# Kernel optimization log

Hardware: AMD Instinct MI355X
Metric: run time of the kernel (lower is better)

The kernel has to match this reference:

```python
import jax, jax.numpy as jnp
import numpy as np

COUNTS = [1536, 8192, 16384, 24576, 12288, 1024, 512, 512, 256, 128, 128]
OFFS = np.concatenate([[0], np.cumsum(COUNTS)]).astype(int).tolist()
N = OFFS[-1]          # 65536 atoms total, sorted by degree
MAX_DEG = 10
BATCH = 2048          # fixed GraphGather batch size
F_IN = 75
GC = 256
DENSE = 512
N_TASKS = 12
N_CLASSES = 2
BN_EPS = 1e-3         # keras BatchNormalization default epsilon


def _graph_conv(x, deg_adjs, w0, wself, wneigh, b):
    # deepchem GraphConv: per-degree (self @ Wself + sum_neighbors @ Wneigh + b), relu
    outs = [x[OFFS[0]:OFFS[1]] @ w0 + b[0]]  # degree-0 atoms: self transform only
    for d in range(1, MAX_DEG + 1):
        self_atoms = x[OFFS[d]:OFFS[d + 1]]            # [n_d, F]
        neigh = x[deg_adjs[d - 1]].sum(axis=1)         # gather [n_d, d, F] -> sum -> [n_d, F]
        outs.append(self_atoms @ wself[d - 1] + neigh @ wneigh[d - 1] + b[d])
    return jax.nn.relu(jnp.concatenate(outs, axis=0))


def _graph_pool(x, deg_adjs):
    # deepchem GraphPool: elementwise max over {self} U neighbors, per degree
    outs = [x[OFFS[0]:OFFS[1]]]  # degree-0 atoms pass through
    for d in range(1, MAX_DEG + 1):
        self_atoms = x[OFFS[d]:OFFS[d + 1]]
        outs.append(jnp.maximum(self_atoms, x[deg_adjs[d - 1]].max(axis=1)))
    return jnp.concatenate(outs, axis=0)


def _bn(x, g, bta, m, v):
    # inference-mode BatchNormalization (training=False -> moving stats)
    return g * (x - m) * jax.lax.rsqrt(v + BN_EPS) + bta


def setup_inputs():
    key = jax.random.key(0)
    ks = iter(jax.random.split(key, 64))
    inp = {}
    inp["atom_features"] = jax.random.normal(next(ks), (N, F_IN), jnp.float32)
    inp["degree_slice"] = jnp.asarray(
        np.stack([np.array(OFFS[:-1]), np.array(COUNTS)], axis=1), jnp.int32)
    # each molecule gets exactly N/BATCH atoms so no GraphGather segment is empty
    inp["membership"] = jax.random.permutation(
        next(ks), jnp.arange(N, dtype=jnp.int32) % BATCH)
    inp["n_samples"] = BATCH
    for d in range(1, MAX_DEG + 1):
        inp["deg_adj_%d" % d] = jax.random.randint(
            next(ks), (COUNTS[d], d), 0, N, jnp.int32)

    def lin(k, fi, fo):
        return jax.random.normal(k, (fi, fo), jnp.float32) * np.float32(1.0 / np.sqrt(fi))

    for li, fi in [(1, F_IN), (2, GC)]:
        inp["gc%d_w0" % li] = lin(next(ks), fi, GC)
        inp["gc%d_wself" % li] = jnp.stack([lin(next(ks), fi, GC) for _ in range(MAX_DEG)])
        inp["gc%d_wneigh" % li] = jnp.stack([lin(next(ks), fi, GC) for _ in range(MAX_DEG)])
        inp["gc%d_b" % li] = jnp.zeros((MAX_DEG + 1, GC), jnp.float32)
    for bi, dim in [(1, GC), (2, GC), (3, DENSE)]:
        inp["bn%d_gamma" % bi] = jnp.ones((dim,), jnp.float32)
        inp["bn%d_beta" % bi] = jnp.zeros((dim,), jnp.float32)
        inp["bn%d_mean" % bi] = jnp.zeros((dim,), jnp.float32)
        inp["bn%d_var" % bi] = jnp.ones((dim,), jnp.float32)
    inp["dense_w"] = lin(next(ks), GC, DENSE)
    inp["dense_b"] = jnp.zeros((DENSE,), jnp.float32)
    inp["out_w"] = lin(next(ks), 2 * DENSE, N_TASKS * N_CLASSES)
    inp["out_b"] = jnp.zeros((N_TASKS * N_CLASSES,), jnp.float32)
    return inp


def reference(atom_features, degree_slice, membership, n_samples,
              deg_adj_1, deg_adj_2, deg_adj_3, deg_adj_4, deg_adj_5,
              deg_adj_6, deg_adj_7, deg_adj_8, deg_adj_9, deg_adj_10,
              gc1_w0, gc1_wself, gc1_wneigh, gc1_b,
              gc2_w0, gc2_wself, gc2_wneigh, gc2_b,
              bn1_gamma, bn1_beta, bn1_mean, bn1_var,
              bn2_gamma, bn2_beta, bn2_mean, bn2_var,
              bn3_gamma, bn3_beta, bn3_mean, bn3_var,
              dense_w, dense_b, out_w, out_b):
    deg_adjs = [deg_adj_1, deg_adj_2, deg_adj_3, deg_adj_4, deg_adj_5,
                deg_adj_6, deg_adj_7, deg_adj_8, deg_adj_9, deg_adj_10]
    h = _graph_conv(atom_features, deg_adjs, gc1_w0, gc1_wself, gc1_wneigh, gc1_b)
    h = _bn(h, bn1_gamma, bn1_beta, bn1_mean, bn1_var)
    h = _graph_pool(h, deg_adjs)
    h = _graph_conv(h, deg_adjs, gc2_w0, gc2_wself, gc2_wneigh, gc2_b)
    h = _bn(h, bn2_gamma, bn2_beta, bn2_mean, bn2_var)
    h = _graph_pool(h, deg_adjs)
    h = jax.nn.relu(h @ dense_w + dense_b)
    h = _bn(h, bn3_gamma, bn3_beta, bn3_mean, bn3_var)
    # GraphGather: tanh(concat(segment_sum, segment_max))
    ssum = jax.ops.segment_sum(h, membership, num_segments=BATCH)
    smax = jax.ops.segment_max(h, membership, num_segments=BATCH)
    fp = jnp.tanh(jnp.concatenate([ssum, smax], axis=1))   # [BATCH, 2*DENSE]
    logits = (fp @ out_w + out_b).reshape(BATCH, N_TASKS, N_CLASSES)[:n_samples]
    probs = jax.nn.softmax(logits, axis=-1)
    return probs, logits, fp
```

## Files before the change

kernel.cpp:

```cpp
#include <hip/hip_runtime.h>
#include <hip/hip_fp16.h>
#include <math.h>

#define NATOMS 65536

typedef _Float16 f16_t;
typedef __attribute__((ext_vector_type(8))) _Float16 half8;
typedef __attribute__((ext_vector_type(4))) float f32x4;

__constant__ int c_offs[12] = {0,1536,9728,26112,50688,62976,64000,64512,65024,65280,65408,65536};

struct Adj { const int* p[10]; };

__device__ __forceinline__ int seg_of(int row) {
    int s = 0;
#pragma unroll
    for (int i = 1; i <= 10; ++i) s += (row >= c_offs[i]) ? 1 : 0;
    return s;
}

__device__ __forceinline__ void glds16(const f16_t* g, f16_t* l) {
    __builtin_amdgcn_global_load_lds(
        (const __attribute__((address_space(1))) unsigned int*)g,
        (__attribute__((address_space(3))) unsigned int*)l,
        16, 0, 0);
}

__device__ __forceinline__ half8 max8(half8 a, half8 b) {
    half8 r;
#pragma unroll
    for (int e = 0; e < 8; ++e) r[e] = (a[e] >= b[e]) ? a[e] : b[e];
    return r;
}


__global__ void pack_cvt(const float* __restrict__ g1w0, const float* __restrict__ g1ws,
                         const float* __restrict__ g1wn,
                         const float* __restrict__ g2w0, const float* __restrict__ g2ws,
                         const float* __restrict__ g2wn,
                         const float* __restrict__ dw, const float* __restrict__ ow,
                         f16_t* __restrict__ W1p, f16_t* __restrict__ W2p,
                         f16_t* __restrict__ Wdp, f16_t* __restrict__ Wop,
                         int* __restrict__ counts,
                         const float* __restrict__ xf, f16_t* __restrict__ xq) {
    if (blockIdx.x >= 8384) {
        int idx = (blockIdx.x - 8384) * 256 + threadIdx.x;
        int r = idx / 12;
        int cc = idx - r * 12;
        int c = cc << 3;
        f16_t o[8];
#pragma unroll
        for (int e = 0; e < 8; ++e)
            o[e] = (c + e < 75) ? (f16_t)xf[(size_t)r*75 + c + e] : (f16_t)0.f;
        *(uint4*)(xq + (size_t)r*96 + c) = *(uint4*)o;
        return;
    }
    int idx = blockIdx.x * 256 + threadIdx.x;
    if (idx < 2048) counts[idx] = 0;
    if (idx < 540672) {
        int j = idx & 7, lane = (idx >> 3) & 63;
        int kb = (idx >> 9) % 6;
        int rest = idx / (512 * 6);
        int ni = rest & 15, s = rest >> 4;
        int k = kb * 32 + (lane >> 4) * 8 + j;
        int n = ni * 16 + (lane & 15);
        float v = 0.f;
        if (k < 75) v = (s == 0) ? g1w0[k*256 + n] : g1ws[((s-1)*75 + k)*256 + n];
        else if (k >= 96 && k < 171 && s > 0) v = g1wn[((s-1)*75 + (k-96))*256 + n];
        W1p[idx] = (f16_t)v;
    } else if (idx < 1982464) {
        int i2 = idx - 540672;
        int j = i2 & 7, lane = (i2 >> 3) & 63;
        int kb = (i2 >> 9) & 15;
        int rest = i2 >> 13;
        int ni = rest & 15, s = rest >> 4;
        int k = kb * 32 + (lane >> 4) * 8 + j;
        int n = ni * 16 + (lane & 15);
        float v = 0.f;
        if (k < 256) v = (s == 0) ? g2w0[k*256 + n] : g2ws[((s-1)*256 + k)*256 + n];
        else if (s > 0) v = g2wn[((s-1)*256 + (k-256))*256 + n];
        W2p[i2] = (f16_t)v;
    } else if (idx < 2113536) {
        int i2 = idx - 1982464;
        int j = i2 & 7, lane = (i2 >> 3) & 63;
        int kb = (i2 >> 9) & 7;
        int ni = (i2 >> 12) & 31;
        int k = kb * 32 + (lane >> 4) * 8 + j;
        int n = ni * 16 + (lane & 15);
        Wdp[i2] = (f16_t)dw[(size_t)k*512 + n];
    } else {
        int i2 = idx - 2113536;
        int j = i2 & 7, lane = (i2 >> 3) & 63;
        int kb = (i2 >> 9) & 31;
        int ni = i2 >> 14;
        int k = kb * 32 + (lane >> 4) * 8 + j;
        int n = ni * 16 + (lane & 15);
        Wop[i2] = (n < 24) ? (f16_t)ow[k*24 + n] : (f16_t)0.f;
    }
}

template<int D, int LD>
__device__ __forceinline__ void gathD(float* v, const f16_t* __restrict__ src,
                                      const int* __restrict__ ap, int c) {
    int rows[D];
#pragma unroll
    for (int j = 0; j < D; ++j) rows[j] = ap[j];
    uint4 raw[D];
#pragma unroll
    for (int j = 0; j < D; ++j) raw[j] = *(const uint4*)(src + (size_t)rows[j]*LD + c);
#pragma unroll
    for (int j = 0; j < D; ++j) {
        const f16_t* u = (const f16_t*)&raw[j];
#pragma unroll
        for (int e = 0; e < 8; ++e) v[e] += (float)u[e];
    }
}

template<int LD>
__device__ __forceinline__ void gath_sum(float* v, const f16_t* __restrict__ src,
                                         const int* __restrict__ ap, int s, int c) {
    switch (s) {
        case 1:  gathD<1,LD>(v,src,ap,c);  break;
        case 2:  gathD<2,LD>(v,src,ap,c);  break;
        case 3:  gathD<3,LD>(v,src,ap,c);  break;
        case 4:  gathD<4,LD>(v,src,ap,c);  break;
        case 5:  gathD<5,LD>(v,src,ap,c);  break;
        case 6:  gathD<6,LD>(v,src,ap,c);  break;
        case 7:  gathD<7,LD>(v,src,ap,c);  break;
        case 8:  gathD<8,LD>(v,src,ap,c);  break;
        case 9:  gathD<9,LD>(v,src,ap,c);  break;
        case 10: gathD<10,LD>(v,src,ap,c); break;
        default: break;
    }
}

template<int D, int LD>
__device__ __forceinline__ void gathD_pk(half8& v, const f16_t* __restrict__ src,
                                         const int* __restrict__ ap, int c) {
    int rows[D];
#pragma unroll
    for (int j = 0; j < D; ++j) rows[j] = ap[j];
    half8 raw[D];
#pragma unroll
    for (int j = 0; j < D; ++j) raw[j] = *(const half8*)(src + (size_t)rows[j]*LD + c);
#pragma unroll
    for (int j = 0; j < D; ++j) v = max8(v, raw[j]);
}

template<int LD>
__device__ __forceinline__ void gath_max(half8& v, const f16_t* __restrict__ src,
                                         const int* __restrict__ ap, int s, int c) {
    switch (s) {
        case 1:  gathD_pk<1,LD>(v,src,ap,c);  break;
        case 2:  gathD_pk<2,LD>(v,src,ap,c);  break;
        case 3:  gathD_pk<3,LD>(v,src,ap,c);  break;
        case 4:  gathD_pk<4,LD>(v,src,ap,c);  break;
        case 5:  gathD_pk<5,LD>(v,src,ap,c);  break;
        case 6:  gathD_pk<6,LD>(v,src,ap,c);  break;
        case 7:  gathD_pk<7,LD>(v,src,ap,c);  break;
        case 8:  gathD_pk<8,LD>(v,src,ap,c);  break;
        case 9:  gathD_pk<9,LD>(v,src,ap,c);  break;
        case 10: gathD_pk<10,LD>(v,src,ap,c); break;
        default: break;
    }
}

__global__ __launch_bounds__(256) void nbsum_sc(const f16_t* __restrict__ xq,
                                                f16_t* __restrict__ NBX, Adj adj,
                                                const int* __restrict__ mem,
                                                int* __restrict__ counts,
                                                int* __restrict__ slots) {
    if (blockIdx.x >= 3072) {
        int i = (blockIdx.x - 3072) * 256 + threadIdx.x;
        int s = mem[i];
        int p = atomicAdd(&counts[s], 1);
        if (p < 32) slots[s*32 + p] = i;
        return;
    }
    int idx = blockIdx.x * 256 + threadIdx.x;
    int r = (int)((unsigned)idx / 12u);
    int cc = idx - r * 12;
    int c = cc << 3;
    int s = seg_of(r);
    float v[8];
#pragma unroll
    for (int e = 0; e < 8; ++e) v[e] = 0.f;
    if (s > 0)
        gath_sum<96>(v, xq, adj.p[s-1] + (size_t)(r - c_offs[s]) * s, s, c);
    f16_t o[8];
#pragma unroll
    for (int e = 0; e < 8; ++e) o[e] = (f16_t)v[e];
    *(uint4*)(NBX + (size_t)(r>>4)*1536 + (c>>5)*512 + ((c>>3)&3)*128 + (r&15)*8) = *(uint4*)o;
}

template<bool BLOB>
__global__ __launch_bounds__(256) void pool_k(const f16_t* __restrict__ H,
                                              f16_t* __restrict__ P, Adj adj) {
    int idx = blockIdx.x * 256 + threadIdx.x;
    int r = idx >> 5;
    int c = (idx & 31) << 3;
    int s = seg_of(r);
    half8 v = *(const half8*)(H + (size_t)r*256 + c);
    if (s > 0)
        gath_max<256>(v, H, adj.p[s-1] + (size_t)(r - c_offs[s]) * s, s, c);
    if (BLOB)
        *(half8*)(P + (size_t)(r>>4)*4096 + (c>>5)*512 + ((c>>3)&3)*128 + (r&15)*8) = v;
    else
        *(half8*)(P + (size_t)r*256 + c) = v;
}

__global__ __launch_bounds__(256) void nbsum_k(const f16_t* __restrict__ P,
                                               f16_t* __restrict__ NB, Adj adj) {
    int idx = blockIdx.x * 256 + threadIdx.x;
    int r = idx >> 5;
    int c = (idx & 31) << 3;
    int s = seg_of(r);
    float v[8];
#pragma unroll
    for (int e = 0; e < 8; ++e) v[e] = 0.f;
    if (s > 0)
        gath_sum<256>(v, P, adj.p[s-1] + (size_t)(r - c_offs[s]) * s, s, c);
    f16_t o[8];
#pragma unroll
    for (int e = 0; e < 8; ++e) o[e] = (f16_t)v[e];
    *(uint4*)(NB + (size_t)(r>>4)*4096 + (c>>5)*512 + ((c>>3)&3)*128 + (r&15)*8) = *(uint4*)o;
}

template<int NKB, int KSPB, int LDA, int NKBA1, int NY, int N, bool SEG>
__global__ __launch_bounds__(512, 2)
void gemm256(const f16_t* __restrict__ A0, const f16_t* __restrict__ A1,
             const f16_t* __restrict__ Wp,
             const float* __restrict__ bias,
             const float* __restrict__ bng, const float* __restrict__ bnb,
             const float* __restrict__ bnm, const float* __restrict__ bnv,
             f16_t* __restrict__ C)
{
    constexpr int NT  = NKB;
    constexpr int NNT = N / 16;
    __shared__ f16_t sm[32768];

    const int t = threadIdx.x;
    const int lane = t & 63, w = t >> 6;
    const int wm = w >> 2, wn = w & 3;
    const int quad = lane >> 4, l16 = lane & 15;
    const int id = blockIdx.x;
    const int xi = id / NY, y = id - xi * NY;
    const int r0 = xi * 256;
    const int n0 = y * 256;
    const int rtg = r0 >> 4;
    const int nbase = n0 >> 4;
    const int segB = SEG ? seg_of(r0) : 0;
    const bool strad = SEG && (seg_of(r0 + 255) != segB);
    const int segw = SEG ? seg_of(r0 + wm*128) : 0;

    f32x4 acc[8][4];
#pragma unroll
    for (int mi = 0; mi < 8; ++mi)
#pragma unroll
        for (int ni = 0; ni < 4; ++ni) acc[mi][ni] = (f32x4){0.f,0.f,0.f,0.f};

    size_t aoff[2];
#pragma unroll
    for (int i = 0; i < 2; ++i)
        aoff[i] = (size_t)(r0 + (w*2 + i)*16 + l16) * LDA + quad*8;

    auto stage = [&](int kb, int buf) {
        f16_t* bb = sm + buf*16384;
#pragma unroll
        for (int i = 0; i < 2; ++i) {
            const int rt = w*2 + i;
            if constexpr (KSPB > 0) {
                if (kb < KSPB)
                    glds16(A0 + (size_t)kb*32 + aoff[i], bb + rt*512);
                else
                    glds16(A1 + ((size_t)(rtg + rt)*NKBA1 + (kb - KSPB))*512 + lane*8,
                           bb + rt*512);
            } else {
                glds16(A1 + ((size_t)(rtg + rt)*NKBA1 + kb)*512 + lane*8,
                       bb + rt*512);
            }
            glds16(Wp + ((size_t)(segB*NNT + nbase + rt)*NKB + kb)*512 + lane*8,
                   bb + 8192 + rt*512);
        }
    };

    stage(0, 0);
    __syncthreads();

    for (int kt = 0; kt < NT; ++kt) {
        const int buf = kt & 1;
        if (kt + 1 < NT) stage(kt + 1, buf ^ 1);
        const f16_t* bb = sm + buf*16384;

        half8 bfr[4];
        if (strad) {
#pragma unroll
            for (int ni = 0; ni < 4; ++ni)
                bfr[ni] = *(const half8*)(Wp +
                    ((size_t)(segw*NNT + nbase + wn*4 + ni)*NKB + kt)*512 + lane*8);
        } else {
#pragma unroll
            for (int ni = 0; ni < 4; ++ni)
                bfr[ni] = *(const half8*)(bb + 8192 + (wn*4 + ni)*512 + lane*8);
        }

#pragma unroll
        for (int ph = 0; ph < 4; ++ph) {
            half8 a[2];
#pragma unroll
            for (int m2 = 0; m2 < 2; ++m2)
                a[m2] = *(const half8*)(bb + (wm*8 + ph*2 + m2)*512 + lane*8);
#pragma unroll
            for (int m2 = 0; m2 < 2; ++m2)
#pragma unroll
                for (int ni = 0; ni < 4; ++ni)
                    acc[ph*2 + m2][ni] = __builtin_amdgcn_mfma_f32_16x16x32_f16(
                        a[m2], bfr[ni], acc[ph*2 + m2][ni], 0, 0, 0);
        }
        __syncthreads();
    }

    f16_t* eps = sm;
#pragma unroll
    for (int s = 0; s < 4; ++s) {
        if (wm == (s >> 1)) {
#pragma unroll
            for (int ni = 0; ni < 4; ++ni) {
                const int lcol = wn*64 + ni*16 + l16;
                const int col = n0 + lcol;
                const float scale = bng[col] * rsqrtf(bnv[col] + 1e-3f);
                const float shift = bnb[col] - bnm[col] * scale;
                const float bv = bias[(SEG ? segw*N : 0) + col];
#pragma unroll
                for (int m2 = 0; m2 < 4; ++m2) {
                    const int mi = (s & 1)*4 + m2;
                    const int rowb = m2*16 + quad*4;
#pragma unroll
                    for (int rr = 0; rr < 4; ++rr) {
                        float v = acc[mi][ni][rr] + bv;
                        v = fmaxf(v, 0.f);
                        v = fmaf(v, scale, shift);
                        eps[(rowb + rr)*264 + lcol] = (f16_t)v;
                    }
                }
            }
        }
        __syncthreads();
#pragma unroll
        for (int k = 0; k < 4; ++k) {
            int idx = k*512 + t;
            int row = idx >> 5, ch = idx & 31;
            *(uint4*)(C + (size_t)(r0 + s*64 + row)*N + n0 + ch*8) =
                *(const uint4*)&eps[row*264 + ch*8];
        }
        __syncthreads();
    }
}

__global__ __launch_bounds__(256, 2)
void gemm_dir(const f16_t* __restrict__ A, const f16_t* __restrict__ Wp,
              const float* __restrict__ bias,
              const float* __restrict__ bng, const float* __restrict__ bnb,
              const float* __restrict__ bnm, const float* __restrict__ bnv,
              f16_t* __restrict__ C)
{
    constexpr int NKB = 8, N = 512;
    __shared__ f16_t eps[128*136];
    const int t = threadIdx.x, lane = t & 63, w = t >> 6;
    const int wm = w >> 1, wn = w & 1;
    const int quad = lane >> 4, l16 = lane & 15;
    const int id = blockIdx.x;
    const int xcd = id & 7;
    const int j = id >> 3;
    const int xi = xcd * 64 + (j >> 2);
    const int y = j & 3;
    const int r0 = xi * 128, n0 = y * 128;
    const int rt0 = (r0 >> 4) + wm*4;
    const int nt0 = (n0 >> 4) + wn*4;

    f32x4 acc[4][4];
#pragma unroll
    for (int mi = 0; mi < 4; ++mi)
#pragma unroll
        for (int ni = 0; ni < 4; ++ni) acc[mi][ni] = (f32x4){0.f,0.f,0.f,0.f};

    const f16_t* ap = A  + (size_t)rt0 * NKB * 512 + lane*8;
    const f16_t* bp = Wp + (size_t)nt0 * NKB * 512 + lane*8;

    half8 aA[4], bA[4], aB[4], bB[4];
#pragma unroll
    for (int i = 0; i < 4; ++i) {
        aA[i] = *(const half8*)(ap + ((size_t)i*NKB + 0)*512);
        bA[i] = *(const half8*)(bp + ((size_t)i*NKB + 0)*512);
    }
#pragma unroll
    for (int kb = 0; kb < NKB; kb += 2) {
        if (kb + 1 < NKB) {
#pragma unroll
            for (int i = 0; i < 4; ++i) {
                aB[i] = *(const half8*)(ap + ((size_t)i*NKB + kb + 1)*512);
                bB[i] = *(const half8*)(bp + ((size_t)i*NKB + kb + 1)*512);
            }
        }
#pragma unroll
        for (int mi = 0; mi < 4; ++mi)
#pragma unroll
            for (int ni = 0; ni < 4; ++ni)
                acc[mi][ni] = __builtin_amdgcn_mfma_f32_16x16x32_f16(
                    aA[mi], bA[ni], acc[mi][ni], 0, 0, 0);
        if (kb + 2 < NKB) {
#pragma unroll
            for (int i = 0; i < 4; ++i) {
                aA[i] = *(const half8*)(ap + ((size_t)i*NKB + kb + 2)*512);
                bA[i] = *(const half8*)(bp + ((size_t)i*NKB + kb + 2)*512);
            }
        }
        if (kb + 1 < NKB) {
#pragma unroll
            for (int mi = 0; mi < 4; ++mi)
#pragma unroll
                for (int ni = 0; ni < 4; ++ni)
                    acc[mi][ni] = __builtin_amdgcn_mfma_f32_16x16x32_f16(
                        aB[mi], bB[ni], acc[mi][ni], 0, 0, 0);
        }
    }

#pragma unroll
    for (int ni = 0; ni < 4; ++ni) {
        const int lcol = wn*64 + ni*16 + l16;
        const int col = n0 + lcol;
        const float scale = bng[col] * rsqrtf(bnv[col] + 1e-3f);
        const float shift = bnb[col] - bnm[col] * scale;
        const float bv = bias[col];
#pragma unroll
        for (int mi = 0; mi < 4; ++mi) {
            const int rowb = wm*64 + mi*16 + quad*4;
#pragma unroll
            for (int rr = 0; rr < 4; ++rr) {
                float v = acc[mi][ni][rr] + bv;
                v = fmaxf(v, 0.f);
                v = fmaf(v, scale, shift);
                eps[(rowb + rr)*136 + lcol] = (f16_t)v;
            }
        }
    }
    __syncthreads();
#pragma unroll
    for (int k2 = 0; k2 < 8; ++k2) {
        int idx = k2*256 + t;
        int row = idx >> 4, ch = idx & 15;
        *(uint4*)(C + (size_t)(r0 + row)*N + n0 + ch*8) =
            *(const uint4*)&eps[row*136 + ch*8];
    }
}

__global__ __launch_bounds__(256)
void reduce_k(const f16_t* __restrict__ H3, const int* __restrict__ slots,
              float* __restrict__ fp) {
    __shared__ float shs[3][512];
    __shared__ float shm[3][512];
    int s = blockIdx.x;
    int t = threadIdx.x;
    int w = t >> 6, l = t & 63;
    int c = l * 8;
    const int* sl = slots + s*32 + w*8;
    float sm[8], mx[8];
#pragma unroll
    for (int e = 0; e < 8; ++e) { sm[e] = 0.f; mx[e] = -INFINITY; }
#pragma unroll
    for (int i = 0; i < 8; ++i) {
        int a = sl[i];
        uint4 raw = *(const uint4*)(H3 + (size_t)a*512 + c);
        const f16_t* u = (const f16_t*)&raw;
#pragma unroll
        for (int e = 0; e < 8; ++e) {
            float f = (float)u[e];
            sm[e] += f;
            mx[e] = fmaxf(mx[e], f);
        }
    }
    if (w) {
        *(float4*)&shs[w-1][c]   = *(float4*)&sm[0];
        *(float4*)&shs[w-1][c+4] = *(float4*)&sm[4];
        *(float4*)&shm[w-1][c]   = *(float4*)&mx[0];
        *(float4*)&shm[w-1][c+4] = *(float4*)&mx[4];
    }
    __syncthreads();
    if (w == 0) {
#pragma unroll
        for (int j = 0; j < 3; ++j)
#pragma unroll
            for (int e = 0; e < 8; ++e) {
                sm[e] += shs[j][c+e];
                mx[e] = fmaxf(mx[e], shm[j][c+e]);
            }
        float o1[8], o2[8];
#pragma unroll
        for (int e = 0; e < 8; ++e) {
            o1[e] = tanhf(sm[e]); o2[e] = tanhf(mx[e]);
        }
        float* fr = fp + (size_t)s*1024;
        *(float4*)(fr + c)       = *(float4*)&o1[0];
        *(float4*)(fr + c + 4)   = *(float4*)&o1[4];
        *(float4*)(fr + 512 + c)     = *(float4*)&o2[0];
        *(float4*)(fr + 512 + c + 4) = *(float4*)&o2[4];
    }
}

__global__ __launch_bounds__(64)
void final_mfma(const float* __restrict__ fp, const f16_t* __restrict__ Wop,
                const float* __restrict__ out_b,
                float* __restrict__ probs, float* __restrict__ logits) {
    const int t = threadIdx.x;
    const int lane = t & 63;
    const int quad = lane >> 4, l16 = lane & 15;
    const int r0 = blockIdx.x * 16;

    f32x4 acc[2];
#pragma unroll
    for (int ni = 0; ni < 2; ++ni) acc[ni] = (f32x4){0.f,0.f,0.f,0.f};

    const size_t rowoff = (size_t)(r0 + l16) * 1024 + quad*8;
    size_t boff[2];
#pragma unroll
    for (int ni = 0; ni < 2; ++ni)
        boff[ni] = (size_t)ni * 32 * 512 + lane*8;

    auto loadA = [&](half8& a, int kb) {
        const float* src = fp + rowoff + kb*32;
        float4 u0 = *(const float4*)(src);
        float4 u1 = *(const float4*)(src + 4);
        half8 h;
        h[0] = (f16_t)u0.x; h[1] = (f16_t)u0.y; h[2] = (f16_t)u0.z; h[3] = (f16_t)u0.w;
        h[4] = (f16_t)u1.x; h[5] = (f16_t)u1.y; h[6] = (f16_t)u1.z; h[7] = (f16_t)u1.w;
        a = h;
    };
    auto loadB = [&](half8* b, int kb) {
#pragma unroll
        for (int ni = 0; ni < 2; ++ni) b[ni] = *(const half8*)(Wop + boff[ni] + (size_t)kb*512);
    };
    auto domfma = [&](half8& a, half8* b) {
#pragma unroll
        for (int ni = 0; ni < 2; ++ni)
            acc[ni] = __builtin_amdgcn_mfma_f32_16x16x32_f16(a, b[ni], acc[ni], 0, 0, 0);
    };

    half8 a0, b0[2], a1, b1[2];
    loadA(a0, 0); loadB(b0, 0);
#pragma unroll
    for (int kb = 0; kb < 32; kb += 2) {
        loadA(a1, kb + 1); loadB(b1, kb + 1);
        domfma(a0, b0);
        if (kb + 2 < 32) { loadA(a0, kb + 2); loadB(b0, kb + 2); }
        domfma(a1, b1);
    }

#pragma unroll
    for (int ni = 0; ni < 2; ++ni) {
        const int c = ni*16 + l16;
        const bool ok = (c < 24);
        const float bv = ok ? out_b[c] : 0.f;
#pragma unroll
        for (int r = 0; r < 4; ++r) {
            float lg = acc[ni][r] + bv;
            float lp = __shfl_xor(lg, 1);
            float m = fmaxf(lg, lp);
            float e  = expf(lg - m);
            float ep = expf(lp - m);
            float pr = e / (e + ep);
            if (ok) {
                int row = r0 + quad*4 + r;
                logits[(size_t)row*24 + c] = lg;
                probs[(size_t)row*24 + c]  = pr;
            }
        }
    }
}

extern "C" void kernel_launch(void* const* d_in, const int* in_sizes, int n_in,
                              void* d_out, int out_size, void* d_ws, size_t ws_size,
                              hipStream_t stream) {
    const float* atom       = (const float*)d_in[0];
    const int*   membership = (const int*)  d_in[2];
    Adj adj;
    for (int d = 0; d < 10; ++d) adj.p[d] = (const int*)d_in[4+d];
    const float* gc1_w0     = (const float*)d_in[14];
    const float* gc1_wself  = (const float*)d_in[15];
    const float* gc1_wneigh = (const float*)d_in[16];
    const float* gc1_b      = (const float*)d_in[17];
    const float* gc2_w0     = (const float*)d_in[18];
    const float* gc2_wself  = (const float*)d_in[19];
    const float* gc2_wneigh = (const float*)d_in[20];
    const float* gc2_b      = (const float*)d_in[21];
    const float* bn1g = (const float*)d_in[22]; const float* bn1b = (const float*)d_in[23];
    const float* bn1m = (const float*)d_in[24]; const float* bn1v = (const float*)d_in[25];
    const float* bn2g = (const float*)d_in[26]; const float* bn2b = (const float*)d_in[27];
    const float* bn2m = (const float*)d_in[28]; const float* bn2v = (const float*)d_in[29];
    const float* bn3g = (const float*)d_in[30]; const float* bn3b = (const float*)d_in[31];
    const float* bn3m = (const float*)d_in[32]; const float* bn3v = (const float*)d_in[33];
    const float* dense_w = (const float*)d_in[34];
    const float* dense_b = (const float*)d_in[35];
    const float* out_w   = (const float*)d_in[36];
    const float* out_b   = (const float*)d_in[37];

    f16_t* wsb = (f16_t*)d_ws;
    f16_t* xq    = wsb;
    f16_t* NBX   = wsb + 6291456;
    f16_t* H1b   = wsb + 12582912;
    f16_t* P1rm  = wsb + 29360128;
    f16_t* NB2b  = wsb + 46137344;
    f16_t* H2b   = H1b;
    f16_t* P2bl  = NB2b;
    f16_t* H3b   = H1b;
    f16_t* W1p   = wsb + 62914560;
    f16_t* W2p   = wsb + 63455232;
    f16_t* Wdp   = wsb + 64897024;
    f16_t* Wop   = wsb + 65028096;
    int*  counts = (int*)(wsb + 65060864);
    int*  slots  = counts + 2048;

    float* outp   = (float*)d_out;
    float* probs  = outp;
    float* logits = outp + 49152;
    float* fp     = outp + 98304;

    pack_cvt<<<11456, 256, 0, stream>>>(gc1_w0, gc1_wself, gc1_wneigh,
                                        gc2_w0, gc2_wself, gc2_wneigh,
                                        dense_w, out_w,
                                        W1p, W2p, Wdp, Wop, counts,
                                        atom, xq);

    nbsum_sc<<<3328, 256, 0, stream>>>(xq, NBX, adj, membership, counts, slots);
    gemm256<6,3,96,3,1,256,true><<<256, 512, 0, stream>>>(
        xq, NBX, W1p, gc1_b, bn1g, bn1b, bn1m, bn1v, H1b);
    pool_k<false><<<(NATOMS*32)/256, 256, 0, stream>>>(H1b, P1rm, adj);

    nbsum_k<<<(NATOMS*32)/256, 256, 0, stream>>>(P1rm, NB2b, adj);
    gemm256<16,8,256,8,1,256,true><<<256, 512, 0, stream>>>(
        P1rm, NB2b, W2p, gc2_b, bn2g, bn2b, bn2m, bn2v, H2b);
    pool_k<true><<<(NATOMS*32)/256, 256, 0, stream>>>(H2b, P2bl, adj);

    gemm_dir<<<2048, 256, 0, stream>>>(
        P2bl, Wdp, dense_b, bn3g, bn3b, bn3m, bn3v, H3b);

    reduce_k<<<2048, 256, 0, stream>>>(H3b, slots, fp);

    final_mfma<<<128, 64, 0, stream>>>(fp, Wop, out_b, probs, logits);
}
```

Before: 338.5 us.

## Replace LDS-staged 256x256 graph-conv GEMM with direct-register 128x128 tiles

Both graph-conv GEMMs switch from a 512-thread kernel with 256x256 tiles, double-buffered through LDS via global_load_lds, to a 256-thread kernel with 128x128 tiles. Each wave now loads its A and B fragments straight from global memory into registers, double-buffered in registers. Blocks are mapped by XCD so neighbouring row tiles share an L2. Because every degree-segment boundary is a multiple of 128, a tile never spans two segments, so the per-wave weight reload path for straddling tiles goes away. The cost is more global and L2 traffic, since operands are no longer shared through LDS across waves.

```diff
diff --git a/kernel.cpp b/kernel.cpp
--- a/kernel.cpp
+++ b/kernel.cpp
@@ -17,13 +17,6 @@
 #pragma unroll
     for (int i = 1; i <= 10; ++i) s += (row >= c_offs[i]) ? 1 : 0;
     return s;
-}
-
-__device__ __forceinline__ void glds16(const f16_t* g, f16_t* l) {
-    __builtin_amdgcn_global_load_lds(
-        (const __attribute__((address_space(1))) unsigned int*)g,
-        (__attribute__((address_space(3))) unsigned int*)l,
-        16, 0, 0);
 }
 
 __device__ __forceinline__ half8 max8(half8 a, half8 b) {
@@ -226,134 +219,106 @@
     *(uint4*)(NB + (size_t)(r>>4)*4096 + (c>>5)*512 + ((c>>3)&3)*128 + (r&15)*8) = *(uint4*)o;
 }
 
-template<int NKB, int KSPB, int LDA, int NKBA1, int NY, int N, bool SEG>
-__global__ __launch_bounds__(512, 2)
-void gemm256(const f16_t* __restrict__ A0, const f16_t* __restrict__ A1,
+template<int NKB, int KSPB, int LDA, int NKBA1, int N, bool SEG>
+__global__ __launch_bounds__(256, 2)
+void gemm_gc(const f16_t* __restrict__ A0, const f16_t* __restrict__ A1,
              const f16_t* __restrict__ Wp,
              const float* __restrict__ bias,
              const float* __restrict__ bng, const float* __restrict__ bnb,
              const float* __restrict__ bnm, const float* __restrict__ bnv,
              f16_t* __restrict__ C)
 {
-    constexpr int NT  = NKB;
     constexpr int NNT = N / 16;
-    __shared__ f16_t sm[32768];
-
-    const int t = threadIdx.x;
-    const int lane = t & 63, w = t >> 6;
-    const int wm = w >> 2, wn = w & 3;
+    constexpr int NYL = N / 128;
+    __shared__ f16_t eps[128*136];
+    const int t = threadIdx.x, lane = t & 63, w = t >> 6;
+    const int wm = w >> 1, wn = w & 1;
     const int quad = lane >> 4, l16 = lane & 15;
     const int id = blockIdx.x;
-    const int xi = id / NY, y = id - xi * NY;
-    const int r0 = xi * 256;
-    const int n0 = y * 256;
-    const int rtg = r0 >> 4;
-    const int nbase = n0 >> 4;
-    const int segB = SEG ? seg_of(r0) : 0;
-    const bool strad = SEG && (seg_of(r0 + 255) != segB);
-    const int segw = SEG ? seg_of(r0 + wm*128) : 0;
-
-    f32x4 acc[8][4];
-#pragma unroll
-    for (int mi = 0; mi < 8; ++mi)
+    const int xcd = id & 7;
+    const int j = id >> 3;
+    const int xi = xcd * 64 + j / NYL;
+    const int y = j % NYL;
+    const int r0 = xi * 128, n0 = y * 128;
+    const int rt0 = (r0 >> 4) + wm*4;
+    const int nt0 = (n0 >> 4) + wn*4;
+    const int seg = SEG ? seg_of(r0) : 0;
+
+    f32x4 acc[4][4];
+#pragma unroll
+    for (int mi = 0; mi < 4; ++mi)
 #pragma unroll
         for (int ni = 0; ni < 4; ++ni) acc[mi][ni] = (f32x4){0.f,0.f,0.f,0.f};
 
-    size_t aoff[2];
-#pragma unroll
-    for (int i = 0; i < 2; ++i)
-        aoff[i] = (size_t)(r0 + (w*2 + i)*16 + l16) * LDA + quad*8;
-
-    auto stage = [&](int kb, int buf) {
-        f16_t* bb = sm + buf*16384;
-#pragma unroll
-        for (int i = 0; i < 2; ++i) {
-            const int rt = w*2 + i;
-            if constexpr (KSPB > 0) {
-                if (kb < KSPB)
-                    glds16(A0 + (size_t)kb*32 + aoff[i], bb + rt*512);
-                else
-                    glds16(A1 + ((size_t)(rtg + rt)*NKBA1 + (kb - KSPB))*512 + lane*8,
-                           bb + rt*512);
-            } else {
-                glds16(A1 + ((size_t)(rtg + rt)*NKBA1 + kb)*512 + lane*8,
-                       bb + rt*512);
+    const f16_t* bpW = Wp + ((size_t)(seg*NNT + nt0) * NKB) * 512 + lane*8;
+    const f16_t* apB = A1 + (size_t)rt0 * NKBA1 * 512 + lane*8;
+    const f16_t* apR = A0 + (size_t)(r0 + wm*64 + l16) * LDA + quad*8;
+
+    auto loadA = [&](half8& dst, int mi, int kb) {
+        if (kb < KSPB)
+            dst = *(const half8*)(apR + (size_t)(mi*16) * LDA + kb*32);
+        else
+            dst = *(const half8*)(apB + ((size_t)mi*NKBA1 + (kb - KSPB))*512);
+    };
+    auto loadB = [&](half8& dst, int ni, int kb) {
+        dst = *(const half8*)(bpW + ((size_t)ni*NKB + kb)*512);
+    };
+
+    half8 aA[4], bA[4], aB[4], bB[4];
+#pragma unroll
+    for (int i = 0; i < 4; ++i) { loadA(aA[i], i, 0); loadB(bA[i], i, 0); }
+#pragma unroll
+    for (int kb = 0; kb < NKB; kb += 2) {
+        if (kb + 1 < NKB) {
+#pragma unroll
+            for (int i = 0; i < 4; ++i) { loadA(aB[i], i, kb + 1); loadB(bB[i], i, kb + 1); }
+        }
+#pragma unroll
+        for (int mi = 0; mi < 4; ++mi)
+#pragma unroll
+            for (int ni = 0; ni < 4; ++ni)
+                acc[mi][ni] = __builtin_amdgcn_mfma_f32_16x16x32_f16(
+                    aA[mi], bA[ni], acc[mi][ni], 0, 0, 0);
+        if (kb + 2 < NKB) {
+#pragma unroll
+            for (int i = 0; i < 4; ++i) { loadA(aA[i], i, kb + 2); loadB(bA[i], i, kb + 2); }
+        }
+        if (kb + 1 < NKB) {
+#pragma unroll
+            for (int mi = 0; mi < 4; ++mi)
+#pragma unroll
+                for (int ni = 0; ni < 4; ++ni)
+                    acc[mi][ni] = __builtin_amdgcn_mfma_f32_16x16x32_f16(
+                        aB[mi], bB[ni], acc[mi][ni], 0, 0, 0);
+        }
+    }
+
+#pragma unroll
+    for (int ni = 0; ni < 4; ++ni) {
+        const int lcol = wn*64 + ni*16 + l16;
+        const int col = n0 + lcol;
+        const float scale = bng[col] * rsqrtf(bnv[col] + 1e-3f);
+        const float shift = bnb[col] - bnm[col] * scale;
+        const float bv = bias[(SEG ? seg*N : 0) + col];
+#pragma unroll
+        for (int mi = 0; mi < 4; ++mi) {
+            const int rowb = wm*64 + mi*16 + quad*4;
+#pragma unroll
+            for (int rr = 0; rr < 4; ++rr) {
+                float v = acc[mi][ni][rr] + bv;
+                v = fmaxf(v, 0.f);
+                v = fmaf(v, scale, shift);
+                eps[(rowb + rr)*136 + lcol] = (f16_t)v;
             }
-            glds16(Wp + ((size_t)(segB*NNT + nbase + rt)*NKB + kb)*512 + lane*8,
-                   bb + 8192 + rt*512);
-        }
-    };
-
-    stage(0, 0);
+        }
+    }
     __syncthreads();
-
-    for (int kt = 0; kt < NT; ++kt) {
-        const int buf = kt & 1;
-        if (kt + 1 < NT) stage(kt + 1, buf ^ 1);
-        const f16_t* bb = sm + buf*16384;
-
-        half8 bfr[4];
-        if (strad) {
-#pragma unroll
-            for (int ni = 0; ni < 4; ++ni)
-                bfr[ni] = *(const half8*)(Wp +
-                    ((size_t)(segw*NNT + nbase + wn*4 + ni)*NKB + kt)*512 + lane*8);
-        } else {
-#pragma unroll
-            for (int ni = 0; ni < 4; ++ni)
-                bfr[ni] = *(const half8*)(bb + 8192 + (wn*4 + ni)*512 + lane*8);
-        }
-
-#pragma unroll
-        for (int ph = 0; ph < 4; ++ph) {
-            half8 a[2];
-#pragma unroll
-            for (int m2 = 0; m2 < 2; ++m2)
-                a[m2] = *(const half8*)(bb + (wm*8 + ph*2 + m2)*512 + lane*8);
-#pragma unroll
-            for (int m2 = 0; m2 < 2; ++m2)
-#pragma unroll
-                for (int ni = 0; ni < 4; ++ni)
-                    acc[ph*2 + m2][ni] = __builtin_amdgcn_mfma_f32_16x16x32_f16(
-                        a[m2], bfr[ni], acc[ph*2 + m2][ni], 0, 0, 0);
-        }
-        __syncthreads();
-    }
-
-    f16_t* eps = sm;
-#pragma unroll
-    for (int s = 0; s < 4; ++s) {
-        if (wm == (s >> 1)) {
-#pragma unroll
-            for (int ni = 0; ni < 4; ++ni) {
-                const int lcol = wn*64 + ni*16 + l16;
-                const int col = n0 + lcol;
-                const float scale = bng[col] * rsqrtf(bnv[col] + 1e-3f);
-                const float shift = bnb[col] - bnm[col] * scale;
-                const float bv = bias[(SEG ? segw*N : 0) + col];
-#pragma unroll
-                for (int m2 = 0; m2 < 4; ++m2) {
-                    const int mi = (s & 1)*4 + m2;
-                    const int rowb = m2*16 + quad*4;
-#pragma unroll
-                    for (int rr = 0; rr < 4; ++rr) {
-                        float v = acc[mi][ni][rr] + bv;
-                        v = fmaxf(v, 0.f);
-                        v = fmaf(v, scale, shift);
-                        eps[(rowb + rr)*264 + lcol] = (f16_t)v;
-                    }
-                }
-            }
-        }
-        __syncthreads();
-#pragma unroll
-        for (int k = 0; k < 4; ++k) {
-            int idx = k*512 + t;
-            int row = idx >> 5, ch = idx & 31;
-            *(uint4*)(C + (size_t)(r0 + s*64 + row)*N + n0 + ch*8) =
-                *(const uint4*)&eps[row*264 + ch*8];
-        }
-        __syncthreads();
+#pragma unroll
+    for (int k2 = 0; k2 < 8; ++k2) {
+        int idx = k2*256 + t;
+        int row = idx >> 4, ch = idx & 15;
+        *(uint4*)(C + (size_t)(r0 + row)*N + n0 + ch*8) =
+            *(const uint4*)&eps[row*136 + ch*8];
     }
 }
 
@@ -631,12 +596,12 @@
                                         atom, xq);
 
     nbsum_sc<<<3328, 256, 0, stream>>>(xq, NBX, adj, membership, counts, slots);
-    gemm256<6,3,96,3,1,256,true><<<256, 512, 0, stream>>>(
+    gemm_gc<6,3,96,3,256,true><<<1024, 256, 0, stream>>>(
         xq, NBX, W1p, gc1_b, bn1g, bn1b, bn1m, bn1v, H1b);
     pool_k<false><<<(NATOMS*32)/256, 256, 0, stream>>>(H1b, P1rm, adj);
 
     nbsum_k<<<(NATOMS*32)/256, 256, 0, stream>>>(P1rm, NB2b, adj);
-    gemm256<16,8,256,8,1,256,true><<<256, 512, 0, stream>>>(
+    gemm_gc<16,8,256,8,256,true><<<1024, 256, 0, stream>>>(
         P1rm, NB2b, W2p, gc2_b, bn2g, bn2b, bn2m, bn2v, H2b);
     pool_k<true><<<(NATOMS*32)/256, 256, 0, stream>>>(H2b, P2bl, adj);
 
```

Measured after the change: 338.6 us, median of 3. About the same (+0.0%).
